# Performance work log

Hardware: AMD Instinct MI355X
Metric: run time of the kernel (lower is better)

The kernel has to match this reference:

```python
import jax, jax.numpy as jnp
import numpy as np

B, L, S, DIM, H, DH, DFF = 2, 2048, 2048, 1024, 16, 64, 4096
EPS = 1e-6


def _ln(x, w, b):
    m = jnp.mean(x, axis=-1, keepdims=True)
    v = jnp.mean(jnp.square(x - m), axis=-1, keepdims=True)
    return (x - m) / jnp.sqrt(v + EPS) * w + b


def _mha(q, k, v, mask):
    # q: [B,L,H*DH], k/v: [B,S,H*DH], mask broadcastable to [B,H,L,S], True = masked
    b, l, _ = q.shape
    s = k.shape[1]
    q = q.reshape(b, l, H, DH)
    k = k.reshape(b, s, H, DH)
    v = v.reshape(b, s, H, DH)
    scale = 1.0 / np.sqrt(DH).astype(np.float32)
    attn = jnp.einsum('blhd,bshd->bhls', q, k) * scale
    if mask is not None:
        attn = jnp.where(mask, -jnp.inf, attn)
    attn = jax.nn.softmax(attn, axis=-1)
    out = jnp.einsum('bhls,bshd->blhd', attn, v)
    return out.reshape(b, l, H * DH)


def setup_inputs() -> dict:
    key = jax.random.key(0)
    ks = jax.random.split(key, 12)
    std = 0.02
    inp = {
        'input': jax.random.normal(ks[0], (B, L, DIM), jnp.float32),
        'source': jax.random.normal(ks[1], (B, S, DIM), jnp.float32),
        # source mask: no source positions masked
        'source_mask': jnp.zeros((B, 1, 1, S), bool),
        # causal mask for self-attention (True above diagonal -> masked)
        'mask': jnp.triu(jnp.ones((L, L), bool), 1)[None, None],
        # self-attention
        'ln_self_w': jnp.ones((DIM,), jnp.float32),
        'ln_self_b': jnp.zeros((DIM,), jnp.float32),
        'w_qkv': std * jax.random.normal(ks[2], (DIM, 3 * DIM), jnp.float32),
        'b_qkv': jnp.zeros((3 * DIM,), jnp.float32),
        'w_so': std * jax.random.normal(ks[3], (DIM, DIM), jnp.float32),
        'b_so': jnp.zeros((DIM,), jnp.float32),
        # cross-attention
        'ln_cross_w': jnp.ones((DIM,), jnp.float32),
        'ln_cross_b': jnp.zeros((DIM,), jnp.float32),
        'w_q': std * jax.random.normal(ks[4], (DIM, DIM), jnp.float32),
        'b_q': jnp.zeros((DIM,), jnp.float32),
        'w_kv': std * jax.random.normal(ks[5], (DIM, 2 * DIM), jnp.float32),
        'b_kv': jnp.zeros((2 * DIM,), jnp.float32),
        'w_co': std * jax.random.normal(ks[6], (DIM, DIM), jnp.float32),
        'b_co': jnp.zeros((DIM,), jnp.float32),
        # MLP (1 layer)
        'ln_mlp_w': jnp.ones((DIM,), jnp.float32),
        'ln_mlp_b': jnp.zeros((DIM,), jnp.float32),
        'w_ff1': std * jax.random.normal(ks[7], (DIM, DFF), jnp.float32),
        'b_ff1': jnp.zeros((DFF,), jnp.float32),
        'w_ff2': std * jax.random.normal(ks[8], (DFF, DIM), jnp.float32),
        'b_ff2': jnp.zeros((DIM,), jnp.float32),
    }
    return inp


def reference(input, source, source_mask, mask,
              ln_self_w, ln_self_b, w_qkv, b_qkv, w_so, b_so,
              ln_cross_w, ln_cross_b, w_q, b_q, w_kv, b_kv, w_co, b_co,
              ln_mlp_w, ln_mlp_b, w_ff1, b_ff1, w_ff2, b_ff2):
    x = input
    # self-attention block (pre-LN)
    h = _ln(x, ln_self_w, ln_self_b)
    qkv = h @ w_qkv + b_qkv
    q, k, v = jnp.split(qkv, 3, axis=-1)
    sa = _mha(q, k, v, mask) @ w_so + b_so
    x = x + sa
    # cross-attention block (pre-LN)
    h = _ln(x, ln_cross_w, ln_cross_b)
    q = h @ w_q + b_q
    kv = source @ w_kv + b_kv
    k, v = jnp.split(kv, 2, axis=-1)
    ca = _mha(q, k, v, source_mask) @ w_co + b_co
    x = x + ca
    # feed-forward block (pre-LN), eval mode (no dropout/droppath)
    h = _ln(x, ln_mlp_w, ln_mlp_b)
    ff = jax.nn.gelu(h @ w_ff1 + b_ff1, approximate=False) @ w_ff2 + b_ff2
    x = x + ff
    return x
```

## Files before the change

kernel.cpp:

```cpp
#include <hip/hip_runtime.h>
#include <hip/hip_bf16.h>
#include <math.h>

typedef __bf16 bf16_t;
typedef __bf16 bf16x8 __attribute__((ext_vector_type(8)));
typedef __bf16 bf16x4 __attribute__((ext_vector_type(4)));
typedef float  f32x4  __attribute__((ext_vector_type(4)));

#define DIM   1024
#define NB    2
#define NL    2048
#define NS    2048
#define NH    16
#define NDH   64
#define NDFF  4096

#define DS_READ_B128(dst, addr) \
    asm volatile("ds_read_b128 %0, %1" : "=v"(dst) : "v"(addr))
#define LGKM0_FENCE() do { \
    asm volatile("s_waitcnt lgkmcnt(0)" ::: "memory"); \
    __builtin_amdgcn_sched_barrier(0); } while (0)

__device__ __forceinline__ bf16x8 ld_bf16x8(const bf16_t* p) {
    return *reinterpret_cast<const bf16x8*>(p);
}

__device__ __forceinline__ void gl_lds16(const bf16_t* g, bf16_t* l) {
    __builtin_amdgcn_global_load_lds(
        (const __attribute__((address_space(1))) void*)g,
        (__attribute__((address_space(3))) void*)l, 16, 0, 0);
}

__device__ __forceinline__ unsigned lds_u32(const bf16_t* p) {
    return (unsigned)(uintptr_t)(__attribute__((address_space(3))) const void*)p;
}

__global__ __launch_bounds__(256)
void wconv_kernel(const float* __restrict__ in, bf16_t* __restrict__ out, int K, int N)
{
    __shared__ float tile[32][33];
    int n0 = blockIdx.x * 32, k0 = blockIdx.y * 32;
    int tx = threadIdx.x & 31, ty = threadIdx.x >> 5;
    #pragma unroll
    for (int j = 0; j < 4; ++j)
        tile[ty + 8*j][tx] = in[(size_t)(k0 + ty + 8*j) * N + n0 + tx];
    __syncthreads();
    #pragma unroll
    for (int j = 0; j < 4; ++j)
        out[(size_t)(n0 + ty + 8*j) * K + k0 + tx] = (bf16_t)tile[tx][ty + 8*j];
}

__global__ __launch_bounds__(256)
void f2b_kernel(const float* __restrict__ in, bf16_t* __restrict__ out)
{
    size_t i = ((size_t)blockIdx.x * 256 + threadIdx.x) * 4;
    float4 v = *reinterpret_cast<const float4*>(in + i);
    bf16x4 o = { (bf16_t)v.x, (bf16_t)v.y, (bf16_t)v.z, (bf16_t)v.w };
    *reinterpret_cast<bf16x4*>(out + i) = o;
}

__global__ __launch_bounds__(256)
void ln_kernel(const float* __restrict__ x, const float* __restrict__ wgt,
               const float* __restrict__ bia, bf16_t* __restrict__ out)
{
    int row = blockIdx.x, tid = threadIdx.x;
    float4 xv = reinterpret_cast<const float4*>(x + (size_t)row * DIM)[tid];
    float s1 = xv.x + xv.y + xv.z + xv.w;
    float s2 = xv.x*xv.x + xv.y*xv.y + xv.z*xv.z + xv.w*xv.w;
    #pragma unroll
    for (int off = 32; off > 0; off >>= 1) {
        s1 += __shfl_xor(s1, off, 64);
        s2 += __shfl_xor(s2, off, 64);
    }
    __shared__ float red[8];
    int w = tid >> 6;
    if ((tid & 63) == 0) { red[w] = s1; red[w + 4] = s2; }
    __syncthreads();
    s1 = red[0] + red[1] + red[2] + red[3];
    s2 = red[4] + red[5] + red[6] + red[7];
    float mean = s1 * (1.0f / DIM);
    float var  = s2 * (1.0f / DIM) - mean * mean;
    float rstd = rsqrtf(var + 1e-6f);
    float4 wv = reinterpret_cast<const float4*>(wgt)[tid];
    float4 bv = reinterpret_cast<const float4*>(bia)[tid];
    bf16x4 o = { (bf16_t)((xv.x - mean) * rstd * wv.x + bv.x),
                 (bf16_t)((xv.y - mean) * rstd * wv.y + bv.y),
                 (bf16_t)((xv.z - mean) * rstd * wv.z + bv.z),
                 (bf16_t)((xv.w - mean) * rstd * wv.w + bv.w) };
    reinterpret_cast<bf16x4*>(out + (size_t)row * DIM)[tid] = o;
}

template<int EPI, int BM, int BN>
__global__ __launch_bounds__(256)
void gemm_kernel(const bf16_t* __restrict__ A, const bf16_t* __restrict__ BT,
                 const float* __restrict__ bias, const float* __restrict__ res,
                 void* __restrict__ out, int M, int N, int K)
{
    constexpr int WM = BM / 2, WN = BN / 2;
    constexpr int AM = WM / 16, AN = WN / 16;
    constexpr int ABE = (BM + BN) * 64;
    __shared__ __align__(16) bf16_t lds[2 * ABE];

    int tid = threadIdx.x;
    int lane = tid & 63, w = tid >> 6;
    int wr = w >> 1, wc = w & 1;
    int la = lane & 15, lg = lane >> 4;

    int gx = gridDim.x;
    int flat = blockIdx.y * gx + blockIdx.x;
    int cpx = gx >> 3;
    int xcd = flat & 7, loc = flat >> 3;
    int m0 = (loc / cpx) * BM;
    int n0 = (xcd * cpx + loc % cpx) * BN;

    f32x4 acc[AM][AN] = {};

    int sr  = lane >> 3;
    int sch = lane & 7;
    int scol = ((sch ^ sr) * 8);
    const bf16_t* Ap = A  + (size_t)(m0 + w * (BM / 4) + sr) * K + scol;
    const bf16_t* Bp = BT + (size_t)(n0 + w * (BN / 4) + sr) * K + scol;

    auto stage = [&](int t, int buf) {
        int k0 = t * 64;
        bf16_t* base = &lds[buf * ABE];
        #pragma unroll
        for (int i = 0; i < BM / 32; ++i)
            gl_lds16(Ap + ((size_t)i * 8) * K + k0, base + (w * (BM / 4) + i * 8) * 64);
        #pragma unroll
        for (int i = 0; i < BN / 32; ++i)
            gl_lds16(Bp + ((size_t)i * 8) * K + k0, base + (BM + w * (BN / 4) + i * 8) * 64);
    };

    unsigned ldsb = lds_u32(lds);
    unsigned kla = la & 7;
    unsigned a_base = ldsb + (wr * WM + la) * 128 + ((lg ^ kla) * 16);
    unsigned b_base = ldsb + BM * 128 + (wc * WN + la) * 128 + ((lg ^ kla) * 16);

    auto compute = [&](int buf) {
        unsigned dB = (unsigned)(buf * ABE * 2);
        bf16x8 af[AM], bfr[AN];
        #pragma unroll
        for (int mi = 0; mi < AM; ++mi)
            DS_READ_B128(af[mi], a_base + dB + mi * 2048);
        #pragma unroll
        for (int ni = 0; ni < AN; ++ni)
            DS_READ_B128(bfr[ni], b_base + dB + ni * 2048);
        LGKM0_FENCE();
        __builtin_amdgcn_s_setprio(1);
        #pragma unroll
        for (int mi = 0; mi < AM; ++mi)
            #pragma unroll
            for (int ni = 0; ni < AN; ++ni)
                acc[mi][ni] = __builtin_amdgcn_mfma_f32_16x16x32_bf16(
                                  af[mi], bfr[ni], acc[mi][ni], 0, 0, 0);
        __builtin_amdgcn_s_setprio(0);
        #pragma unroll
        for (int mi = 0; mi < AM; ++mi)
            DS_READ_B128(af[mi], (a_base + dB + mi * 2048) ^ 64u);
        #pragma unroll
        for (int ni = 0; ni < AN; ++ni)
            DS_READ_B128(bfr[ni], (b_base + dB + ni * 2048) ^ 64u);
        LGKM0_FENCE();
        __builtin_amdgcn_s_setprio(1);
        #pragma unroll
        for (int mi = 0; mi < AM; ++mi)
            #pragma unroll
            for (int ni = 0; ni < AN; ++ni)
                acc[mi][ni] = __builtin_amdgcn_mfma_f32_16x16x32_bf16(
                                  af[mi], bfr[ni], acc[mi][ni], 0, 0, 0);
        __builtin_amdgcn_s_setprio(0);
    };

    int nt = K / 64;
    stage(0, 0);
    for (int t = 0; t < nt; ++t) {
        asm volatile("s_waitcnt vmcnt(0)" ::: "memory");
        __builtin_amdgcn_s_barrier();
        __builtin_amdgcn_sched_barrier(0);
        if (t + 1 < nt) stage(t + 1, (t + 1) & 1);
        compute(t & 1);
    }

    #pragma unroll
    for (int mi = 0; mi < AM; ++mi) {
        #pragma unroll
        for (int ni = 0; ni < AN; ++ni) {
            #pragma unroll
            for (int i = 0; i < 4; ++i) {
                int row = m0 + wr * WM + mi * 16 + lg * 4 + i;
                int col = n0 + wc * WN + ni * 16 + la;
                float v = acc[mi][ni][i] + bias[col];
                if (EPI == 1) v = 0.5f * v * (1.0f + erff(v * 0.70710678118f));
                if (EPI == 2)
                    ((float*)out)[(size_t)row * N + col] = res[(size_t)row * N + col] + v;
                else
                    ((bf16_t*)out)[(size_t)row * N + col] = (bf16_t)v;
            }
        }
    }
}

template<bool CAUSAL>
__global__ __launch_bounds__(256)
void attn_kernel(const bf16_t* __restrict__ Q, int qs,
                 const bf16_t* __restrict__ Kp, int ks,
                 const bf16_t* __restrict__ Vp, int vs,
                 bf16_t* __restrict__ O, int os, int L, int S)
{
    __shared__ __align__(16) bf16_t Ks[64 * 64];
    __shared__ __align__(16) bf16_t Vt[64 * 64];
    __shared__ __align__(16) bf16_t Ps[4][32 * 64];

    int tid = threadIdx.x, lane = tid & 63, w = tid >> 6;
    int la = lane & 15, lg = lane >> 4;
    int qtile = (CAUSAL ? (gridDim.x - 1 - blockIdx.x) : blockIdx.x) * 128;
    int b = blockIdx.y >> 4, h = blockIdx.y & 15;

    const bf16_t* qb = Q  + (size_t)(b * L) * qs + h * 64;
    const bf16_t* kb = Kp + (size_t)(b * S) * ks + h * 64;
    const bf16_t* vb = Vp + (size_t)(b * S) * vs + h * 64;
    bf16_t*       ob = O  + (size_t)(b * L) * os + h * 64;

    bf16x8 qf[2][2];
    #pragma unroll
    for (int rg = 0; rg < 2; ++rg) {
        int qrow = qtile + w * 32 + rg * 16 + la;
        qf[rg][0] = ld_bf16x8(qb + (size_t)qrow * qs + lg * 8);
        qf[rg][1] = ld_bf16x8(qb + (size_t)qrow * qs + 32 + lg * 8);
        #pragma unroll
        for (int j = 0; j < 8; ++j) {
            qf[rg][0][j] = qf[rg][0][j] * (bf16_t)0.125f;
            qf[rg][1][j] = qf[rg][1][j] * (bf16_t)0.125f;
        }
    }

    f32x4 zero = {0.f, 0.f, 0.f, 0.f};
    f32x4 o[2][4];
    #pragma unroll
    for (int rg = 0; rg < 2; ++rg)
        #pragma unroll
        for (int dt = 0; dt < 4; ++dt) o[rg][dt] = zero;
    float lpart[2][4] = {};

    int rk  = tid >> 3;
    int ck8 = tid & 7;
    int sv0   = tid & 31;
    int dbase = (tid >> 5) * 8;
    int r7 = la & 7;

    int n_full = (CAUSAL ? qtile : S) / 64;
    int nit = n_full + (CAUSAL ? 2 : 0);

    bf16x8 kr0 = ld_bf16x8(kb + (size_t)rk * ks + ck8 * 8);
    bf16x8 kr1 = ld_bf16x8(kb + (size_t)(rk + 32) * ks + ck8 * 8);
    bf16x8 vr0 = ld_bf16x8(vb + (size_t)sv0 * vs + dbase);
    bf16x8 vr1 = ld_bf16x8(vb + (size_t)(sv0 + 32) * vs + dbase);

    for (int it = 0; it < nit; ++it) {
        int s0 = it * 64;
        bool diag = CAUSAL && (it >= n_full);

        __syncthreads();
        *reinterpret_cast<bf16x8*>(&Ks[rk * 64 + ((ck8 ^ (rk & 7)) * 8)]) = kr0;
        *reinterpret_cast<bf16x8*>(&Ks[(rk + 32) * 64 + ((ck8 ^ (rk & 7)) * 8)]) = kr1;
        #pragma unroll
        for (int j = 0; j < 8; ++j) {
            Vt[(dbase + j) * 64 + (sv0 ^ (j << 3))]        = vr0[j];
            Vt[(dbase + j) * 64 + ((sv0 + 32) ^ (j << 3))] = vr1[j];
        }
        __syncthreads();

        if (it + 1 < nit) {
            int s1 = s0 + 64;
            kr0 = ld_bf16x8(kb + (size_t)(s1 + rk) * ks + ck8 * 8);
            kr1 = ld_bf16x8(kb + (size_t)(s1 + rk + 32) * ks + ck8 * 8);
            vr0 = ld_bf16x8(vb + (size_t)(s1 + sv0) * vs + dbase);
            vr1 = ld_bf16x8(vb + (size_t)(s1 + sv0 + 32) * vs + dbase);
        }

        f32x4 sf[2][4];
        #pragma unroll
        for (int ct = 0; ct < 4; ++ct) {
            const bf16_t* kr = &Ks[(ct * 16 + la) * 64];
            bf16x8 k0 = ld_bf16x8(kr + ((lg ^ r7) * 8));
            bf16x8 k1 = ld_bf16x8(kr + (((4 + lg) ^ r7) * 8));
            #pragma unroll
            for (int rg = 0; rg < 2; ++rg) {
                f32x4 z = zero;
                z = __builtin_amdgcn_mfma_f32_16x16x32_bf16(qf[rg][0], k0, z, 0, 0, 0);
                z = __builtin_amdgcn_mfma_f32_16x16x32_bf16(qf[rg][1], k1, z, 0, 0, 0);
                sf[rg][ct] = z;
            }
        }

        #pragma unroll
        for (int rg = 0; rg < 2; ++rg) {
            #pragma unroll
            for (int ct = 0; ct < 4; ++ct) {
                #pragma unroll
                for (int i = 0; i < 4; ++i) {
                    float p = __expf(sf[rg][ct][i]);
                    if (diag) {
                        int sg = s0 + ct * 16 + la;
                        int qg = qtile + w * 32 + rg * 16 + lg * 4 + i;
                        if (sg > qg) p = 0.f;
                    }
                    lpart[rg][i] += p;
                    int row = rg * 16 + lg * 4 + i;
                    Ps[w][row * 64 + ((ct * 16 + la) ^ ((row & 7) << 3))] = (bf16_t)p;
                }
            }
        }

        bf16x8 pa[2][2];
        #pragma unroll
        for (int rg = 0; rg < 2; ++rg) {
            const bf16_t* pr = &Ps[w][(rg * 16 + la) * 64];
            pa[rg][0] = ld_bf16x8(pr + ((lg ^ r7) * 8));
            pa[rg][1] = ld_bf16x8(pr + (((4 + lg) ^ r7) * 8));
        }
        #pragma unroll
        for (int dt = 0; dt < 4; ++dt) {
            const bf16_t* vr = &Vt[(dt * 16 + la) * 64];
            bf16x8 v0 = ld_bf16x8(vr + ((lg ^ r7) * 8));
            bf16x8 v1 = ld_bf16x8(vr + (((4 + lg) ^ r7) * 8));
            #pragma unroll
            for (int rg = 0; rg < 2; ++rg) {
                o[rg][dt] = __builtin_amdgcn_mfma_f32_16x16x32_bf16(pa[rg][0], v0, o[rg][dt], 0, 0, 0);
                o[rg][dt] = __builtin_amdgcn_mfma_f32_16x16x32_bf16(pa[rg][1], v1, o[rg][dt], 0, 0, 0);
            }
        }
    }

    #pragma unroll
    for (int off = 1; off < 16; off <<= 1)
        #pragma unroll
        for (int rg = 0; rg < 2; ++rg)
            #pragma unroll
            for (int i = 0; i < 4; ++i)
                lpart[rg][i] += __shfl_xor(lpart[rg][i], off, 64);

    #pragma unroll
    for (int rg = 0; rg < 2; ++rg)
        #pragma unroll
        for (int dt = 0; dt < 4; ++dt)
            #pragma unroll
            for (int i = 0; i < 4; ++i) {
                int row = qtile + w * 32 + rg * 16 + lg * 4 + i;
                float val = o[rg][dt][i] / lpart[rg][i];
                ob[(size_t)row * os + dt * 16 + la] = (bf16_t)val;
            }
}

extern "C" void kernel_launch(void* const* d_in, const int* in_sizes, int n_in,
                              void* d_out, int out_size, void* d_ws, size_t ws_size,
                              hipStream_t stream)
{
    const float* input     = (const float*)d_in[0];
    const float* source    = (const float*)d_in[1];
    const float* ln_self_w = (const float*)d_in[4];
    const float* ln_self_b = (const float*)d_in[5];
    const float* w_qkv     = (const float*)d_in[6];
    const float* b_qkv     = (const float*)d_in[7];
    const float* w_so      = (const float*)d_in[8];
    const float* b_so      = (const float*)d_in[9];
    const float* ln_cross_w= (const float*)d_in[10];
    const float* ln_cross_b= (const float*)d_in[11];
    const float* w_q       = (const float*)d_in[12];
    const float* b_q       = (const float*)d_in[13];
    const float* w_kv      = (const float*)d_in[14];
    const float* b_kv      = (const float*)d_in[15];
    const float* w_co      = (const float*)d_in[16];
    const float* b_co      = (const float*)d_in[17];
    const float* ln_mlp_w  = (const float*)d_in[18];
    const float* ln_mlp_b  = (const float*)d_in[19];
    const float* w_ff1     = (const float*)d_in[20];
    const float* b_ff1     = (const float*)d_in[21];
    const float* w_ff2     = (const float*)d_in[22];
    const float* b_ff2     = (const float*)d_in[23];

    const int M = NB * NL;

    char* ws = (char*)d_ws;
    size_t off = 0;
    auto alloc = [&](size_t bytes) { char* p = ws + off; off += (bytes + 255) & ~(size_t)255; return p; };

    bf16_t* wT_qkv = (bf16_t*)alloc((size_t)3072 * 1024 * 2);
    bf16_t* wT_so  = (bf16_t*)alloc((size_t)1024 * 1024 * 2);
    bf16_t* wT_q   = (bf16_t*)alloc((size_t)1024 * 1024 * 2);
    bf16_t* wT_kv  = (bf16_t*)alloc((size_t)2048 * 1024 * 2);
    bf16_t* wT_co  = (bf16_t*)alloc((size_t)1024 * 1024 * 2);
    bf16_t* wT_ff1 = (bf16_t*)alloc((size_t)4096 * 1024 * 2);
    bf16_t* wT_ff2 = (bf16_t*)alloc((size_t)1024 * 4096 * 2);
    bf16_t* srcb   = (bf16_t*)alloc((size_t)M * 1024 * 2);
    bf16_t* hbuf   = (bf16_t*)alloc((size_t)M * 1024 * 2);
    bf16_t* qkvb   = (bf16_t*)alloc((size_t)M * 3072 * 2);
    bf16_t* attnb  = (bf16_t*)alloc((size_t)M * 1024 * 2);
    bf16_t* qcb    = (bf16_t*)alloc((size_t)M * 1024 * 2);
    bf16_t* kvcb   = (bf16_t*)alloc((size_t)M * 2048 * 2);
    float*  xbuf   = (float*) alloc((size_t)M * 1024 * 4);
    bf16_t* ff1b   = (bf16_t*)alloc((size_t)M * 4096 * 2);
    (void)ws_size; (void)n_in; (void)in_sizes; (void)out_size;

    wconv_kernel<<<dim3(3072/32, 1024/32), 256, 0, stream>>>(w_qkv, wT_qkv, 1024, 3072);
    wconv_kernel<<<dim3(1024/32, 1024/32), 256, 0, stream>>>(w_so,  wT_so,  1024, 1024);
    wconv_kernel<<<dim3(1024/32, 1024/32), 256, 0, stream>>>(w_q,   wT_q,   1024, 1024);
    wconv_kernel<<<dim3(2048/32, 1024/32), 256, 0, stream>>>(w_kv,  wT_kv,  1024, 2048);
    wconv_kernel<<<dim3(1024/32, 1024/32), 256, 0, stream>>>(w_co,  wT_co,  1024, 1024);
    wconv_kernel<<<dim3(4096/32, 1024/32), 256, 0, stream>>>(w_ff1, wT_ff1, 1024, 4096);
    wconv_kernel<<<dim3(1024/32, 4096/32), 256, 0, stream>>>(w_ff2, wT_ff2, 4096, 1024);
    f2b_kernel<<<(M * 1024) / (256 * 4), 256, 0, stream>>>(source, srcb);

    ln_kernel<<<M, 256, 0, stream>>>(input, ln_self_w, ln_self_b, hbuf);
    gemm_kernel<0,128,128><<<dim3(3072/128, M/128), 256, 0, stream>>>(hbuf, wT_qkv, b_qkv, nullptr, qkvb, M, 3072, 1024);
    attn_kernel<true><<<dim3(NL/128, NB*NH), 256, 0, stream>>>(qkvb, 3072, qkvb + 1024, 3072, qkvb + 2048, 3072,
                                                               attnb, 1024, NL, NL);
    gemm_kernel<2,128,64><<<dim3(1024/64, M/128), 256, 0, stream>>>(attnb, wT_so, b_so, input, xbuf, M, 1024, 1024);

    ln_kernel<<<M, 256, 0, stream>>>(xbuf, ln_cross_w, ln_cross_b, hbuf);
    gemm_kernel<0,128,64><<<dim3(1024/64, M/128), 256, 0, stream>>>(hbuf, wT_q, b_q, nullptr, qcb, M, 1024, 1024);
    gemm_kernel<0,128,128><<<dim3(2048/128, M/128), 256, 0, stream>>>(srcb, wT_kv, b_kv, nullptr, kvcb, M, 2048, 1024);
    attn_kernel<false><<<dim3(NL/128, NB*NH), 256, 0, stream>>>(qcb, 1024, kvcb, 2048, kvcb + 1024, 2048,
                                                                attnb, 1024, NL, NS);
    gemm_kernel<2,128,64><<<dim3(1024/64, M/128), 256, 0, stream>>>(attnb, wT_co, b_co, xbuf, xbuf, M, 1024, 1024);

    ln_kernel<<<M, 256, 0, stream>>>(xbuf, ln_mlp_w, ln_mlp_b, hbuf);
    gemm_kernel<1,128,128><<<dim3(4096/128, M/128), 256, 0, stream>>>(hbuf, wT_ff1, b_ff1, nullptr, ff1b, M, 4096, 1024);
    gemm_kernel<2,128,64><<<dim3(1024/64, M/128), 256, 0, stream>>>(ff1b, wT_ff2, b_ff2, xbuf, d_out, M, 1024, 4096);
}
```

Measured before the change: 406.1 us.

## Split attention q-tile across eight waves of sixteen rows each

Attention blocks now launch 512 threads: 8 waves each owning 16 query rows instead of 4 waves owning 32. Per-wave register state and per-thread K/V staging loads are halved, and each block has more waves to hide latency. In exchange, each K/V LDS fragment read feeds only one MFMA row group, and barrier cost is spread over less work per wave.

```diff
diff --git a/kernel.cpp b/kernel.cpp
--- a/kernel.cpp
+++ b/kernel.cpp
@@ -202,7 +202,7 @@
 }
 
 template<bool CAUSAL>
-__global__ __launch_bounds__(256)
+__global__ __launch_bounds__(512)
 void attn_kernel(const bf16_t* __restrict__ Q, int qs,
                  const bf16_t* __restrict__ Kp, int ks,
                  const bf16_t* __restrict__ Vp, int vs,
@@ -210,7 +210,7 @@
 {
     __shared__ __align__(16) bf16_t Ks[64 * 64];
     __shared__ __align__(16) bf16_t Vt[64 * 64];
-    __shared__ __align__(16) bf16_t Ps[4][32 * 64];
+    __shared__ __align__(16) bf16_t Ps[8][16 * 64];
 
     int tid = threadIdx.x, lane = tid & 63, w = tid >> 6;
     int la = lane & 15, lg = lane >> 4;
@@ -222,135 +222,104 @@
     const bf16_t* vb = Vp + (size_t)(b * S) * vs + h * 64;
     bf16_t*       ob = O  + (size_t)(b * L) * os + h * 64;
 
-    bf16x8 qf[2][2];
-    #pragma unroll
-    for (int rg = 0; rg < 2; ++rg) {
-        int qrow = qtile + w * 32 + rg * 16 + la;
-        qf[rg][0] = ld_bf16x8(qb + (size_t)qrow * qs + lg * 8);
-        qf[rg][1] = ld_bf16x8(qb + (size_t)qrow * qs + 32 + lg * 8);
-        #pragma unroll
-        for (int j = 0; j < 8; ++j) {
-            qf[rg][0][j] = qf[rg][0][j] * (bf16_t)0.125f;
-            qf[rg][1][j] = qf[rg][1][j] * (bf16_t)0.125f;
-        }
+    int qrow = qtile + w * 16 + la;
+    bf16x8 qf0 = ld_bf16x8(qb + (size_t)qrow * qs + lg * 8);
+    bf16x8 qf1 = ld_bf16x8(qb + (size_t)qrow * qs + 32 + lg * 8);
+    #pragma unroll
+    for (int j = 0; j < 8; ++j) {
+        qf0[j] = qf0[j] * (bf16_t)0.125f;
+        qf1[j] = qf1[j] * (bf16_t)0.125f;
     }
 
     f32x4 zero = {0.f, 0.f, 0.f, 0.f};
-    f32x4 o[2][4];
-    #pragma unroll
-    for (int rg = 0; rg < 2; ++rg)
-        #pragma unroll
-        for (int dt = 0; dt < 4; ++dt) o[rg][dt] = zero;
-    float lpart[2][4] = {};
-
-    int rk  = tid >> 3;
-    int ck8 = tid & 7;
-    int sv0   = tid & 31;
-    int dbase = (tid >> 5) * 8;
+    f32x4 o[4];
+    #pragma unroll
+    for (int dt = 0; dt < 4; ++dt) o[dt] = zero;
+    float lpart[4] = {0.f, 0.f, 0.f, 0.f};
+
+    int rk    = tid >> 3;
+    int ck8   = tid & 7;
+    int sv    = tid & 63;
+    int dbase = (tid >> 6) * 8;
     int r7 = la & 7;
 
     int n_full = (CAUSAL ? qtile : S) / 64;
     int nit = n_full + (CAUSAL ? 2 : 0);
 
-    bf16x8 kr0 = ld_bf16x8(kb + (size_t)rk * ks + ck8 * 8);
-    bf16x8 kr1 = ld_bf16x8(kb + (size_t)(rk + 32) * ks + ck8 * 8);
-    bf16x8 vr0 = ld_bf16x8(vb + (size_t)sv0 * vs + dbase);
-    bf16x8 vr1 = ld_bf16x8(vb + (size_t)(sv0 + 32) * vs + dbase);
+    bf16x8 kr = ld_bf16x8(kb + (size_t)rk * ks + ck8 * 8);
+    bf16x8 vr = ld_bf16x8(vb + (size_t)sv * vs + dbase);
 
     for (int it = 0; it < nit; ++it) {
         int s0 = it * 64;
         bool diag = CAUSAL && (it >= n_full);
 
         __syncthreads();
-        *reinterpret_cast<bf16x8*>(&Ks[rk * 64 + ((ck8 ^ (rk & 7)) * 8)]) = kr0;
-        *reinterpret_cast<bf16x8*>(&Ks[(rk + 32) * 64 + ((ck8 ^ (rk & 7)) * 8)]) = kr1;
-        #pragma unroll
-        for (int j = 0; j < 8; ++j) {
-            Vt[(dbase + j) * 64 + (sv0 ^ (j << 3))]        = vr0[j];
-            Vt[(dbase + j) * 64 + ((sv0 + 32) ^ (j << 3))] = vr1[j];
-        }
+        *reinterpret_cast<bf16x8*>(&Ks[rk * 64 + ((ck8 ^ (rk & 7)) * 8)]) = kr;
+        #pragma unroll
+        for (int j = 0; j < 8; ++j)
+            Vt[(dbase + j) * 64 + (sv ^ (j << 3))] = vr[j];
         __syncthreads();
 
         if (it + 1 < nit) {
             int s1 = s0 + 64;
-            kr0 = ld_bf16x8(kb + (size_t)(s1 + rk) * ks + ck8 * 8);
-            kr1 = ld_bf16x8(kb + (size_t)(s1 + rk + 32) * ks + ck8 * 8);
-            vr0 = ld_bf16x8(vb + (size_t)(s1 + sv0) * vs + dbase);
-            vr1 = ld_bf16x8(vb + (size_t)(s1 + sv0 + 32) * vs + dbase);
-        }
-
-        f32x4 sf[2][4];
+            kr = ld_bf16x8(kb + (size_t)(s1 + rk) * ks + ck8 * 8);
+            vr = ld_bf16x8(vb + (size_t)(s1 + sv) * vs + dbase);
+        }
+
+        f32x4 sf[4];
         #pragma unroll
         for (int ct = 0; ct < 4; ++ct) {
-            const bf16_t* kr = &Ks[(ct * 16 + la) * 64];
-            bf16x8 k0 = ld_bf16x8(kr + ((lg ^ r7) * 8));
-            bf16x8 k1 = ld_bf16x8(kr + (((4 + lg) ^ r7) * 8));
-            #pragma unroll
-            for (int rg = 0; rg < 2; ++rg) {
-                f32x4 z = zero;
-                z = __builtin_amdgcn_mfma_f32_16x16x32_bf16(qf[rg][0], k0, z, 0, 0, 0);
-                z = __builtin_amdgcn_mfma_f32_16x16x32_bf16(qf[rg][1], k1, z, 0, 0, 0);
-                sf[rg][ct] = z;
-            }
-        }
-
-        #pragma unroll
-        for (int rg = 0; rg < 2; ++rg) {
-            #pragma unroll
-            for (int ct = 0; ct < 4; ++ct) {
-                #pragma unroll
-                for (int i = 0; i < 4; ++i) {
-                    float p = __expf(sf[rg][ct][i]);
-                    if (diag) {
-                        int sg = s0 + ct * 16 + la;
-                        int qg = qtile + w * 32 + rg * 16 + lg * 4 + i;
-                        if (sg > qg) p = 0.f;
-                    }
-                    lpart[rg][i] += p;
-                    int row = rg * 16 + lg * 4 + i;
-                    Ps[w][row * 64 + ((ct * 16 + la) ^ ((row & 7) << 3))] = (bf16_t)p;
-                }
-            }
-        }
-
-        bf16x8 pa[2][2];
-        #pragma unroll
-        for (int rg = 0; rg < 2; ++rg) {
-            const bf16_t* pr = &Ps[w][(rg * 16 + la) * 64];
-            pa[rg][0] = ld_bf16x8(pr + ((lg ^ r7) * 8));
-            pa[rg][1] = ld_bf16x8(pr + (((4 + lg) ^ r7) * 8));
-        }
-        #pragma unroll
-        for (int dt = 0; dt < 4; ++dt) {
-            const bf16_t* vr = &Vt[(dt * 16 + la) * 64];
-            bf16x8 v0 = ld_bf16x8(vr + ((lg ^ r7) * 8));
-            bf16x8 v1 = ld_bf16x8(vr + (((4 + lg) ^ r7) * 8));
-            #pragma unroll
-            for (int rg = 0; rg < 2; ++rg) {
-                o[rg][dt] = __builtin_amdgcn_mfma_f32_16x16x32_bf16(pa[rg][0], v0, o[rg][dt], 0, 0, 0);
-                o[rg][dt] = __builtin_amdgcn_mfma_f32_16x16x32_bf16(pa[rg][1], v1, o[rg][dt], 0, 0, 0);
-            }
-        }
-    }
-
-    #pragma unroll
-    for (int off = 1; off < 16; off <<= 1)
-        #pragma unroll
-        for (int rg = 0; rg < 2; ++rg)
-            #pragma unroll
-            for (int i = 0; i < 4; ++i)
-                lpart[rg][i] += __shfl_xor(lpart[rg][i], off, 64);
-
-    #pragma unroll
-    for (int rg = 0; rg < 2; ++rg)
-        #pragma unroll
-        for (int dt = 0; dt < 4; ++dt)
+            const bf16_t* kp = &Ks[(ct * 16 + la) * 64];
+            bf16x8 k0 = ld_bf16x8(kp + ((lg ^ r7) * 8));
+            bf16x8 k1 = ld_bf16x8(kp + (((4 + lg) ^ r7) * 8));
+            f32x4 z = zero;
+            z = __builtin_amdgcn_mfma_f32_16x16x32_bf16(qf0, k0, z, 0, 0, 0);
+            z = __builtin_amdgcn_mfma_f32_16x16x32_bf16(qf1, k1, z, 0, 0, 0);
+            sf[ct] = z;
+        }
+
+        #pragma unroll
+        for (int ct = 0; ct < 4; ++ct) {
             #pragma unroll
             for (int i = 0; i < 4; ++i) {
-                int row = qtile + w * 32 + rg * 16 + lg * 4 + i;
-                float val = o[rg][dt][i] / lpart[rg][i];
-                ob[(size_t)row * os + dt * 16 + la] = (bf16_t)val;
+                float p = __expf(sf[ct][i]);
+                if (diag) {
+                    int sg = s0 + ct * 16 + la;
+                    int qg = qtile + w * 16 + lg * 4 + i;
+                    if (sg > qg) p = 0.f;
+                }
+                lpart[i] += p;
+                int row = lg * 4 + i;
+                Ps[w][row * 64 + ((ct * 16 + la) ^ ((row & 7) << 3))] = (bf16_t)p;
             }
+        }
+
+        bf16x8 pa0 = ld_bf16x8(&Ps[w][la * 64 + ((lg ^ r7) * 8)]);
+        bf16x8 pa1 = ld_bf16x8(&Ps[w][la * 64 + (((4 + lg) ^ r7) * 8)]);
+        #pragma unroll
+        for (int dt = 0; dt < 4; ++dt) {
+            const bf16_t* vp = &Vt[(dt * 16 + la) * 64];
+            bf16x8 v0 = ld_bf16x8(vp + ((lg ^ r7) * 8));
+            bf16x8 v1 = ld_bf16x8(vp + (((4 + lg) ^ r7) * 8));
+            o[dt] = __builtin_amdgcn_mfma_f32_16x16x32_bf16(pa0, v0, o[dt], 0, 0, 0);
+            o[dt] = __builtin_amdgcn_mfma_f32_16x16x32_bf16(pa1, v1, o[dt], 0, 0, 0);
+        }
+    }
+
+    #pragma unroll
+    for (int off = 1; off < 16; off <<= 1)
+        #pragma unroll
+        for (int i = 0; i < 4; ++i)
+            lpart[i] += __shfl_xor(lpart[i], off, 64);
+
+    #pragma unroll
+    for (int dt = 0; dt < 4; ++dt)
+        #pragma unroll
+        for (int i = 0; i < 4; ++i) {
+            int row = qtile + w * 16 + lg * 4 + i;
+            float val = o[dt][i] / lpart[i];
+            ob[(size_t)row * os + dt * 16 + la] = (bf16_t)val;
+        }
 }
 
 extern "C" void kernel_launch(void* const* d_in, const int* in_sizes, int n_in,
@@ -414,14 +383,14 @@
 
     ln_kernel<<<M, 256, 0, stream>>>(input, ln_self_w, ln_self_b, hbuf);
     gemm_kernel<0,128,128><<<dim3(3072/128, M/128), 256, 0, stream>>>(hbuf, wT_qkv, b_qkv, nullptr, qkvb, M, 3072, 1024);
-    attn_kernel<true><<<dim3(NL/128, NB*NH), 256, 0, stream>>>(qkvb, 3072, qkvb + 1024, 3072, qkvb + 2048, 3072,
+    attn_kernel<true><<<dim3(NL/128, NB*NH), 512, 0, stream>>>(qkvb, 3072, qkvb + 1024, 3072, qkvb + 2048, 3072,
                                                                attnb, 1024, NL, NL);
     gemm_kernel<2,128,64><<<dim3(1024/64, M/128), 256, 0, stream>>>(attnb, wT_so, b_so, input, xbuf, M, 1024, 1024);
 
     ln_kernel<<<M, 256, 0, stream>>>(xbuf, ln_cross_w, ln_cross_b, hbuf);
     gemm_kernel<0,128,64><<<dim3(1024/64, M/128), 256, 0, stream>>>(hbuf, wT_q, b_q, nullptr, qcb, M, 1024, 1024);
     gemm_kernel<0,128,128><<<dim3(2048/128, M/128), 256, 0, stream>>>(srcb, wT_kv, b_kv, nullptr, kvcb, M, 2048, 1024);
-    attn_kernel<false><<<dim3(NL/128, NB*NH), 256, 0, stream>>>(qcb, 1024, kvcb, 2048, kvcb + 1024, 2048,
+    attn_kernel<false><<<dim3(NL/128, NB*NH), 512, 0, stream>>>(qcb, 1024, kvcb, 2048, kvcb + 1024, 2048,
                                                                 attnb, 1024, NL, NS);
     gemm_kernel<2,128,64><<<dim3(1024/64, M/128), 256, 0, stream>>>(attnb, wT_co, b_co, xbuf, xbuf, M, 1024, 1024);
 
```

After: 391.1 us. 1.04x faster.
